# Kernel optimization log

Hardware: AMD Instinct MI355X
Metric: run time of the kernel (lower is better)

The kernel has to match this reference:

```python
import jax, jax.numpy as jnp
import numpy as np

K = 64                 # count_bins
HID = 32               # hidden width of conditioner MLP
PARAM_DIM = 4 * K - 1  # widths(K) + heights(K) + derivs(K-1) + lambdas(K)
BOUND = 3.0
MIN_BIN_W = 1e-3
MIN_BIN_H = 1e-3
MIN_DERIV = 1e-3
N = 1_048_576


def setup_inputs() -> dict:
    key = jax.random.key(0)
    ks = jax.random.split(key, 5)

    def init_lin(k, fan_in, fan_out):
        bnd = 1.0 / np.sqrt(fan_in)
        kw, kb = jax.random.split(k)
        W = jax.random.uniform(kw, (fan_in, fan_out), jnp.float32, -bnd, bnd)
        b = jax.random.uniform(kb, (fan_out,), jnp.float32, -bnd, bnd)
        return W, b

    W1, b1 = init_lin(ks[0], 1, HID)
    W2, b2 = init_lin(ks[1], HID, HID)
    W3, b3 = init_lin(ks[2], HID, PARAM_DIM)
    x = jax.random.normal(ks[3], (N,), jnp.float32)
    condx = jax.random.normal(ks[4], (N,), jnp.float32)
    return {"x": x, "condx": condx, "W1": W1, "b1": b1,
            "W2": W2, "b2": b2, "W3": W3, "b3": b3}


def _normalize_bins(un, min_frac, n):
    # softmax widths -> cumulative knots on [-BOUND, BOUND]
    w = min_frac + (1.0 - min_frac * K) * jax.nn.softmax(un, axis=-1)
    cum = jnp.concatenate([jnp.zeros((n, 1), un.dtype), jnp.cumsum(w, -1)], -1)
    cum = 2.0 * BOUND * cum - BOUND
    cum = cum.at[:, 0].set(-BOUND).at[:, -1].set(BOUND)
    return cum, cum[:, 1:] - cum[:, :-1]


def _spline(x, params):
    # monotonic linear-rational spline (pyro order='linear'), elementwise on x
    n = x.shape[0]
    w_un = params[:, :K]
    h_un = params[:, K:2 * K]
    d_un = params[:, 2 * K:3 * K - 1]
    l_un = params[:, 3 * K - 1:]

    cumw, bw = _normalize_bins(w_un, MIN_BIN_W, n)   # knots/widths in x
    cumh, bh = _normalize_bins(h_un, MIN_BIN_H, n)   # knots/heights in y

    one = jnp.ones((n, 1), x.dtype)
    derivs = jnp.concatenate(
        [one, MIN_DERIV + jax.nn.softplus(d_un), one], -1)  # [n, K+1]
    lambdas = 0.95 * jax.nn.sigmoid(l_un) + 0.025            # [n, K]

    inside = (x >= -BOUND) & (x <= BOUND)
    xc = jnp.clip(x, -BOUND, BOUND)
    # bin search: index of bin containing xc
    idx = jnp.clip(jnp.sum(xc[:, None] >= cumw, axis=-1) - 1, 0, K - 1)[:, None]

    g = lambda a, i: jnp.take_along_axis(a, i, axis=-1)[:, 0]
    xk, wk = g(cumw, idx), g(bw, idx)
    yk, hk = g(cumh, idx), g(bh, idx)
    d0, d1 = g(derivs, idx), g(derivs, idx + 1)
    lam = g(lambdas, idx)

    slope = hk / wk
    wb = jnp.sqrt(d0 / d1)                                   # wa == 1
    wc = (lam * d0 + (1.0 - lam) * wb * d1) / slope
    ya, yb = yk, yk + hk
    yc = ((1.0 - lam) * ya + lam * wb * yb) / ((1.0 - lam) + lam * wb)

    theta = (xc - xk) / wk
    left = theta <= lam
    num = jnp.where(left, ya * (lam - theta) + wc * yc * theta,
                    wc * yc * (1.0 - theta) + wb * yb * (theta - lam))
    den = jnp.where(left, (lam - theta) + wc * theta,
                    wc * (1.0 - theta) + wb * (theta - lam))
    y_in = num / den
    dnum = jnp.where(left, wc * lam * (yc - ya),
                     wb * wc * (1.0 - lam) * (yb - yc))
    ld_in = jnp.log(dnum) - 2.0 * jnp.log(jnp.abs(den)) - jnp.log(wk)

    y = jnp.where(inside, y_in, x)       # identity outside support
    ld = jnp.where(inside, ld_in, 0.0)
    return y, ld


def reference(x, condx, W1, b1, W2, b2, W3, b3):
    # conditioner MLP: cond scalar -> 4K-1 unnormalized spline params
    h = jax.nn.relu(condx[:, None] @ W1 + b1)
    h = jax.nn.relu(h @ W2 + b2)
    params = h @ W3 + b3                 # [N, 4K-1]
    y, logdet = _spline(x, params)
    return y, logdet
```

## Files before the change

### kernel.cpp

```cpp
#include <hip/hip_runtime.h>
#include <math.h>

#define BOUND 3.0f
#define LOG2E 1.4426950408889634f
#define LN2 0.6931471805599453f
#define CINV 0.17806267806267807f

typedef _Float16 half8 __attribute__((ext_vector_type(8)));
typedef _Float16 half4 __attribute__((ext_vector_type(4)));
typedef _Float16 half2v __attribute__((ext_vector_type(2)));
typedef float f32x4 __attribute__((ext_vector_type(4)));

__device__ __forceinline__ float fexp2(float x) { return __builtin_amdgcn_exp2f(x); }
__device__ __forceinline__ float flog2(float x) { return __builtin_amdgcn_logf(x); }
__device__ __forceinline__ float frcp(float x)  { return __builtin_amdgcn_rcpf(x); }

__device__ __forceinline__ float hsum2(half2v a, float c) {
    const half2v ones = {(_Float16)1.f, (_Float16)1.f};
    return __builtin_amdgcn_fdot2(a, ones, c, false);
}

__global__ void prep_kernel(const float* __restrict__ W2, const float* __restrict__ W3,
                            const float* __restrict__ b3,
                            _Float16* __restrict__ aW2, _Float16* __restrict__ aW3,
                            float* __restrict__ b3s) {
    int tid = blockIdx.x * blockDim.x + threadIdx.x;
    int nth = gridDim.x * blockDim.x;
    for (int i = tid; i < 16 * 64 * 8; i += nth) {
        int t = i & 7, l = (i >> 3) & 63, m = i >> 9;
        int k = 8 * (l >> 4) + t, col = 16 * m + (l & 15);
        float v = (col < 255) ? W3[k * 255 + col] : 0.f;
        if (m < 8) v *= LOG2E;
        aW3[i] = (_Float16)v;
    }
    for (int i = tid; i < 2 * 64 * 8; i += nth) {
        int t = i & 7, l = (i >> 3) & 63, m = i >> 9;
        int k = 8 * (l >> 4) + t, col = 16 * m + (l & 15);
        aW2[i] = (_Float16)W2[k * 32 + col];
    }
    for (int i = tid; i < 255; i += nth)
        b3s[i] = b3[i] * ((i < 128) ? LOG2E : 1.f);
}

__global__ __launch_bounds__(64, 2) void spline_kernel(
    const float* __restrict__ x_in, const float* __restrict__ cond_in,
    const float* __restrict__ W1, const float* __restrict__ b1,
    const float* __restrict__ b2, const float* __restrict__ b3s,
    const _Float16* __restrict__ aW2, const _Float16* __restrict__ aW3,
    float* __restrict__ out, int N) {

    __shared__ float sbuf[64 * 64];
    __shared__ float scx[64];

    const int l = threadIdx.x;
    const int j = l & 15, g = l >> 4;
    const int sx = l & 7;
    const int ksw = j & 7;
    const int gown = blockIdx.x * 64 + l;
    const int ic = (gown < N) ? gown : (N - 1);

    float* buf = sbuf;
    _Float16* bufh = (_Float16*)sbuf;

    scx[l] = cond_in[ic];
    float x = x_in[ic];

    float4 w1a = *(const float4*)(W1 + 8 * g);
    float4 w1b = *(const float4*)(W1 + 8 * g + 4);
    float4 b1a = *(const float4*)(b1 + 8 * g);
    float4 b1b = *(const float4*)(b1 + 8 * g + 4);

    half8 h1hi[4], h1lo[4];
#pragma unroll
    for (int n = 0; n < 4; n++) {
        float c = scx[16 * n + j];
        float h[8];
        h[0] = fmaxf(fmaf(c, w1a.x, b1a.x), 0.f);
        h[1] = fmaxf(fmaf(c, w1a.y, b1a.y), 0.f);
        h[2] = fmaxf(fmaf(c, w1a.z, b1a.z), 0.f);
        h[3] = fmaxf(fmaf(c, w1a.w, b1a.w), 0.f);
        h[4] = fmaxf(fmaf(c, w1b.x, b1b.x), 0.f);
        h[5] = fmaxf(fmaf(c, w1b.y, b1b.y), 0.f);
        h[6] = fmaxf(fmaf(c, w1b.z, b1b.z), 0.f);
        h[7] = fmaxf(fmaf(c, w1b.w, b1b.w), 0.f);
#pragma unroll
        for (int t = 0; t < 8; t++) {
            _Float16 hi = (_Float16)h[t];
            h1hi[n][t] = hi;
            h1lo[n][t] = (_Float16)(h[t] - (float)hi);
        }
    }

    half8 a2[2];
    a2[0] = *(const half8*)(aW2 + (0 * 64 + l) * 8);
    a2[1] = *(const half8*)(aW2 + (1 * 64 + l) * 8);

#pragma unroll
    for (int m = 0; m < 2; m++) {
        float4 bb = *(const float4*)(b2 + 16 * m + 4 * g);
        f32x4 binit = {bb.x, bb.y, bb.z, bb.w};
#pragma unroll
        for (int n = 0; n < 4; n++) {
            f32x4 acc = binit;
            acc = __builtin_amdgcn_mfma_f32_16x16x32_f16(a2[m], h1lo[n], acc, 0, 0, 0);
            acc = __builtin_amdgcn_mfma_f32_16x16x32_f16(a2[m], h1hi[n], acc, 0, 0, 0);
            float v0 = fmaxf(acc[0], 0.f), v1 = fmaxf(acc[1], 0.f);
            float v2 = fmaxf(acc[2], 0.f), v3 = fmaxf(acc[3], 0.f);
            _Float16 p0 = (_Float16)v0, p1 = (_Float16)v1, p2 = (_Float16)v2, p3 = (_Float16)v3;
            half4 hv = {p0, p1, p2, p3};
            half4 lv = {(_Float16)(v0 - (float)p0), (_Float16)(v1 - (float)p1),
                        (_Float16)(v2 - (float)p2), (_Float16)(v3 - (float)p3)};
            int rb = (16 * n + j) * 64;
            *(half4*)(bufh + rb + (((2 * m + (g >> 1)) ^ ksw) << 3) + ((g & 1) << 2)) = hv;
            *(half4*)(bufh + rb + (((4 + 2 * m + (g >> 1)) ^ ksw) << 3) + ((g & 1) << 2)) = lv;
        }
    }

    half8 bhi[4], blo[4];
#pragma unroll
    for (int n = 0; n < 4; n++) {
        int rb = (16 * n + j) * 64;
        bhi[n] = *(const half8*)(bufh + rb + ((g ^ ksw) << 3));
        blo[n] = *(const half8*)(bufh + rb + (((4 + g) ^ ksw) << 3));
    }

    bool inside = (x >= -BOUND) && (x <= BOUND);
    float xc = fminf(fmaxf(x, -BOUND), BOUND);

#pragma unroll
    for (int m = 0; m < 4; m++) {
        half8 a = *(const half8*)(aW3 + (m * 64 + l) * 8);
        float4 bb = *(const float4*)(b3s + 16 * m + 4 * g);
        f32x4 binit = {bb.x, bb.y, bb.z, bb.w};
#pragma unroll
        for (int n = 0; n < 4; n++) {
            f32x4 acc = binit;
            acc = __builtin_amdgcn_mfma_f32_16x16x32_f16(a, blo[n], acc, 0, 0, 0);
            acc = __builtin_amdgcn_mfma_f32_16x16x32_f16(a, bhi[n], acc, 0, 0, 0);
            f32x4 e = {fexp2(acc[0]), fexp2(acc[1]), fexp2(acc[2]), fexp2(acc[3])};
            *(f32x4*)(buf + (16 * n + j) * 64 + (((4 * m + g) ^ ksw) << 2)) = e;
        }
    }

    int idx; float idxf, xk, wk;
    {
        f32x4 wv[16];
#pragma unroll
        for (int t = 0; t < 16; t++)
            wv[t] = *(const f32x4*)(buf + l * 64 + (((t ^ sx)) << 2));
        float G[16];
        float run = 0.f;
#pragma unroll
        for (int t = 0; t < 16; t++) {
            run += (wv[t][0] + wv[t][1]) + (wv[t][2] + wv[t][3]);
            G[t] = run;
        }
        float tot = G[15];
        float rcptot = frcp(tot);
        float rr = (xc + BOUND) * tot * CINV;
        float dr1 = 0.0010683761f * tot;
        float dr4 = 4.f * dr1;
        float r = rr, Gsel = 0.f;
        int qidx = 0;
#pragma unroll
        for (int t = 0; t < 15; t++) {
            r -= dr4;
            bool c = (G[t] <= r);
            qidx += c ? 1 : 0;
            Gsel = c ? G[t] : Gsel;
        }
        f32x4 fv = wv[0];
#pragma unroll
        for (int t = 1; t < 16; t++) fv = (qidx == t) ? wv[t] : fv;
        float e0 = fv[0], e1 = fv[1], e2 = fv[2], e3 = fv[3];
        float qf = (float)qidx;
        float rq = fmaf(-qf, dr4, rr);
        float p1 = Gsel + e0, p2 = p1 + e1, p3 = p2 + e2;
        bool c1 = (p1 <= rq - dr1);
        bool c2 = (p2 <= fmaf(-2.f, dr1, rq));
        bool c3 = (p3 <= fmaf(-3.f, dr1, rq));
        idx = 4 * qidx + (c1 ? 1 : 0) + (c2 ? 1 : 0) + (c3 ? 1 : 0);
        float Pk = c1 ? p1 : Gsel; Pk = c2 ? p2 : Pk; Pk = c3 ? p3 : Pk;
        float ek = c1 ? e1 : e0;   ek = c2 ? e2 : ek; ek = c3 ? e3 : ek;
        idxf = (float)idx;
        xk = fmaf(0.006f, idxf, -BOUND) + 5.616f * Pk * rcptot;
        wk = fmaf(5.616f * rcptot, ek, 0.006f);
        wk = (idx == 63) ? (BOUND - xk) : wk;
    }

#pragma unroll
    for (int m = 0; m < 4; m++) {
        half8 a = *(const half8*)(aW3 + ((m + 4) * 64 + l) * 8);
        float4 bb = *(const float4*)(b3s + 64 + 16 * m + 4 * g);
        f32x4 binit = {bb.x, bb.y, bb.z, bb.w};
#pragma unroll
        for (int n = 0; n < 4; n++) {
            f32x4 acc = binit;
            acc = __builtin_amdgcn_mfma_f32_16x16x32_f16(a, bhi[n], acc, 0, 0, 0);
            half4 e = {(_Float16)fexp2(acc[0]), (_Float16)fexp2(acc[1]),
                       (_Float16)fexp2(acc[2]), (_Float16)fexp2(acc[3])};
            *(half4*)(bufh + (16 * n + j) * 64 +
                      (((2 * m + (g >> 1)) ^ ksw) << 3) + ((g & 1) << 2)) = e;
        }
    }

    float yk, hk;
    {
        int qh = idx >> 2, rh = idx & 3;
        float toth = 0.f, Gq = 0.f;
#pragma unroll
        for (int t = 0; t < 8; t++) {
            half8 hv = *(const half8*)(bufh + l * 64 + ((t ^ sx) << 3));
            half2v* hp = (half2v*)&hv;
            float gs0 = hsum2(hp[0], hsum2(hp[1], 0.f));
            float gs1 = hsum2(hp[2], hsum2(hp[3], 0.f));
            toth += gs0 + gs1;
            Gq += (2 * t < qh) ? gs0 : 0.f;
            Gq += (2 * t + 1 < qh) ? gs1 : 0.f;
        }
        half4 fv = *(const half4*)(bufh + l * 64 + (((qh >> 1) ^ sx) << 3) + ((qh & 1) << 2));
        float f0 = (float)fv[0], f1 = (float)fv[1], f2 = (float)fv[2], f3 = (float)fv[3];
        float Sh = Gq;
        Sh += (rh >= 1) ? f0 : 0.f;
        Sh += (rh >= 2) ? f1 : 0.f;
        Sh += (rh >= 3) ? f2 : 0.f;
        float x01 = (rh & 1) ? f1 : f0;
        float x23 = (rh & 1) ? f3 : f2;
        float eidx = (rh & 2) ? x23 : x01;
        float chh = 5.616f * frcp(toth);
        yk = fmaf(0.006f, idxf, -BOUND) + chh * Sh;
        hk = fmaf(chh, eidx, 0.006f);
        hk = (idx == 63) ? (BOUND - yk) : hk;
    }

    int c0 = (idx > 0) ? (idx - 1) : 0;
    float accd0, accd1, accl;
    {
#pragma unroll
        for (int m = 0; m < 4; m++) {
            half8 a = *(const half8*)(aW3 + ((m + 8) * 64 + l) * 8);
#pragma unroll
            for (int n = 0; n < 4; n++) {
                f32x4 acc = {0.f, 0.f, 0.f, 0.f};
                acc = __builtin_amdgcn_mfma_f32_16x16x32_f16(a, bhi[n], acc, 0, 0, 0);
                *(f32x4*)(buf + (16 * n + j) * 64 + (((4 * m + g) ^ ksw) << 2)) = acc;
            }
        }
        accd0 = buf[l * 64 + (((c0 >> 2) ^ sx) << 2) + (c0 & 3)];
        accd1 = buf[l * 64 + (((idx >> 2) ^ sx) << 2) + (idx & 3)];
        float acl0 = buf[l * 64 + ((15 ^ sx) << 2) + 3];
#pragma unroll
        for (int m = 0; m < 4; m++) {
            half8 a = *(const half8*)(aW3 + ((m + 12) * 64 + l) * 8);
#pragma unroll
            for (int n = 0; n < 4; n++) {
                f32x4 acc = {0.f, 0.f, 0.f, 0.f};
                acc = __builtin_amdgcn_mfma_f32_16x16x32_f16(a, bhi[n], acc, 0, 0, 0);
                *(f32x4*)(buf + (16 * n + j) * 64 + (((4 * m + g) ^ ksw) << 2)) = acc;
            }
        }
        float aclB = buf[l * 64 + (((c0 >> 2) ^ sx) << 2) + (c0 & 3)];
        accd0 += b3s[127 + idx];
        accd1 += b3s[(idx < 63) ? (128 + idx) : 191];
        accl = ((idx == 0) ? acl0 : aclB) + b3s[191 + idx];
    }

    float e0t = fexp2(-fabsf(accd0) * LOG2E);
    float sp0 = fmaxf(accd0, 0.f) + LN2 * flog2(1.f + e0t);
    float e1t = fexp2(-fabsf(accd1) * LOG2E);
    float sp1 = fmaxf(accd1, 0.f) + LN2 * flog2(1.f + e1t);
    float d0 = (idx == 0)  ? 1.f : (0.001f + sp0);
    float d1 = (idx == 63) ? 1.f : (0.001f + sp1);
    float sig = frcp(1.f + fexp2(-accl * LOG2E));
    float lam = fmaf(0.95f, sig, 0.025f);

    float rwk = frcp(wk);
    float wb = sqrtf(d0 * frcp(d1));
    float wc = fmaf(lam, d0, (1.f - lam) * wb * d1) * wk * frcp(hk);
    float ya = yk, yb = yk + hk;
    float yc = fmaf(1.f - lam, ya, lam * wb * yb) * frcp(fmaf(lam, wb, 1.f - lam));
    float theta = (xc - xk) * rwk;
    bool left = theta <= lam;
    float num = left ? fmaf(ya, lam - theta, wc * yc * theta)
                     : fmaf(wc * yc, 1.f - theta, wb * yb * (theta - lam));
    float den = left ? fmaf(wc, theta, lam - theta)
                     : fmaf(wc, 1.f - theta, wb * (theta - lam));
    float y_in = num * frcp(den);
    float dnum = left ? (wc * lam * (yc - ya))
                      : (wb * wc * (1.f - lam) * (yb - yc));
    float ld_in = LN2 * (flog2(dnum) - 2.f * flog2(fabsf(den)) - flog2(wk));

    if (gown < N) {
        out[gown]     = inside ? y_in : x;
        out[N + gown] = inside ? ld_in : 0.f;
    }
}

extern "C" void kernel_launch(void* const* d_in, const int* in_sizes, int n_in,
                              void* d_out, int out_size, void* d_ws, size_t ws_size,
                              hipStream_t stream) {
    const float* x  = (const float*)d_in[0];
    const float* cx = (const float*)d_in[1];
    const float* W1 = (const float*)d_in[2];
    const float* b1 = (const float*)d_in[3];
    const float* W2 = (const float*)d_in[4];
    const float* b2 = (const float*)d_in[5];
    const float* W3 = (const float*)d_in[6];
    const float* b3 = (const float*)d_in[7];
    int N = in_sizes[0];

    _Float16* aW3 = (_Float16*)d_ws;
    _Float16* aW2 = aW3 + 16 * 64 * 8;
    float* b3s = (float*)(aW2 + 2 * 64 * 8);
    float* out = (float*)d_out;

    hipLaunchKernelGGL(prep_kernel, dim3(8), dim3(256), 0, stream, W2, W3, b3, aW2, aW3, b3s);
    hipLaunchKernelGGL(spline_kernel, dim3((N + 63) / 64), dim3(64), 0, stream,
                       x, cx, W1, b1, b2, b3s, aW2, aW3, out, N);
}
```

Baseline: 64.28 us.

## Halve shared staging buffer and raise occupancy to four waves per SIMD

Shrinks the per-block shared-memory staging buffer from 64x64 to 64x32 floats by processing the third-layer MFMA outputs in two or four half-width passes and reading each half back before it is overwritten. The cond broadcast now uses a wave shuffle instead of shared memory. Launch bounds are raised from 2 to 4 waves to improve latency hiding. In exchange there are extra LDS round trips and selects, and the tighter register budget may cause spills, since wv[16] now stays live across the passes.

```diff
diff --git a/kernel.cpp b/kernel.cpp
--- a/kernel.cpp
+++ b/kernel.cpp
@@ -42,15 +42,14 @@
         b3s[i] = b3[i] * ((i < 128) ? LOG2E : 1.f);
 }
 
-__global__ __launch_bounds__(64, 2) void spline_kernel(
+__global__ __launch_bounds__(64, 4) void spline_kernel(
     const float* __restrict__ x_in, const float* __restrict__ cond_in,
     const float* __restrict__ W1, const float* __restrict__ b1,
     const float* __restrict__ b2, const float* __restrict__ b3s,
     const _Float16* __restrict__ aW2, const _Float16* __restrict__ aW3,
     float* __restrict__ out, int N) {
 
-    __shared__ float sbuf[64 * 64];
-    __shared__ float scx[64];
+    __shared__ float sbuf[64 * 32];
 
     const int l = threadIdx.x;
     const int j = l & 15, g = l >> 4;
@@ -62,7 +61,7 @@
     float* buf = sbuf;
     _Float16* bufh = (_Float16*)sbuf;
 
-    scx[l] = cond_in[ic];
+    float cx = cond_in[ic];
     float x = x_in[ic];
 
     float4 w1a = *(const float4*)(W1 + 8 * g);
@@ -73,7 +72,7 @@
     half8 h1hi[4], h1lo[4];
 #pragma unroll
     for (int n = 0; n < 4; n++) {
-        float c = scx[16 * n + j];
+        float c = __shfl(cx, 16 * n + j, 64);
         float h[8];
         h[0] = fmaxf(fmaf(c, w1a.x, b1a.x), 0.f);
         h[1] = fmaxf(fmaf(c, w1a.y, b1a.y), 0.f);
@@ -127,27 +126,31 @@
     bool inside = (x >= -BOUND) && (x <= BOUND);
     float xc = fminf(fmaxf(x, -BOUND), BOUND);
 
-#pragma unroll
-    for (int m = 0; m < 4; m++) {
-        half8 a = *(const half8*)(aW3 + (m * 64 + l) * 8);
-        float4 bb = *(const float4*)(b3s + 16 * m + 4 * g);
-        f32x4 binit = {bb.x, bb.y, bb.z, bb.w};
-#pragma unroll
-        for (int n = 0; n < 4; n++) {
-            f32x4 acc = binit;
-            acc = __builtin_amdgcn_mfma_f32_16x16x32_f16(a, blo[n], acc, 0, 0, 0);
-            acc = __builtin_amdgcn_mfma_f32_16x16x32_f16(a, bhi[n], acc, 0, 0, 0);
-            f32x4 e = {fexp2(acc[0]), fexp2(acc[1]), fexp2(acc[2]), fexp2(acc[3])};
-            *(f32x4*)(buf + (16 * n + j) * 64 + (((4 * m + g) ^ ksw) << 2)) = e;
-        }
+    f32x4 wv[16];
+#pragma unroll
+    for (int s = 0; s < 2; s++) {
+#pragma unroll
+        for (int mm = 0; mm < 2; mm++) {
+            int m = 2 * s + mm;
+            half8 a = *(const half8*)(aW3 + (m * 64 + l) * 8);
+            float4 bb = *(const float4*)(b3s + 16 * m + 4 * g);
+            f32x4 binit = {bb.x, bb.y, bb.z, bb.w};
+#pragma unroll
+            for (int n = 0; n < 4; n++) {
+                f32x4 acc = binit;
+                acc = __builtin_amdgcn_mfma_f32_16x16x32_f16(a, blo[n], acc, 0, 0, 0);
+                acc = __builtin_amdgcn_mfma_f32_16x16x32_f16(a, bhi[n], acc, 0, 0, 0);
+                f32x4 e = {fexp2(acc[0]), fexp2(acc[1]), fexp2(acc[2]), fexp2(acc[3])};
+                *(f32x4*)(buf + (16 * n + j) * 32 + (((4 * mm + g) ^ ksw) << 2)) = e;
+            }
+        }
+#pragma unroll
+        for (int t = 0; t < 8; t++)
+            wv[8 * s + t] = *(const f32x4*)(buf + l * 32 + ((t ^ sx) << 2));
     }
 
     int idx; float idxf, xk, wk;
     {
-        f32x4 wv[16];
-#pragma unroll
-        for (int t = 0; t < 16; t++)
-            wv[t] = *(const f32x4*)(buf + l * 64 + (((t ^ sx)) << 2));
         float G[16];
         float run = 0.f;
 #pragma unroll
@@ -233,37 +236,41 @@
         hk = (idx == 63) ? (BOUND - yk) : hk;
     }
 
-    int c0 = (idx > 0) ? (idx - 1) : 0;
-    float accd0, accd1, accl;
-    {
-#pragma unroll
-        for (int m = 0; m < 4; m++) {
-            half8 a = *(const half8*)(aW3 + ((m + 8) * 64 + l) * 8);
+    const int c0 = (idx > 0) ? (idx - 1) : 0;
+    const int rc0a = (c0 < 32) ? c0 : 31;
+    const int rc0b = (c0 >= 32) ? (c0 - 32) : 0;
+    const int rc1a = (idx < 32) ? idx : 31;
+    const int rc1b = (idx >= 32) ? (idx - 32) : 0;
+    float v0a, v0b, v1a, v1b, vl191, vla, vlb;
+#pragma unroll
+    for (int s = 0; s < 4; s++) {
+#pragma unroll
+        for (int mm = 0; mm < 2; mm++) {
+            half8 a = *(const half8*)(aW3 + ((8 + 2 * s + mm) * 64 + l) * 8);
 #pragma unroll
             for (int n = 0; n < 4; n++) {
                 f32x4 acc = {0.f, 0.f, 0.f, 0.f};
                 acc = __builtin_amdgcn_mfma_f32_16x16x32_f16(a, bhi[n], acc, 0, 0, 0);
-                *(f32x4*)(buf + (16 * n + j) * 64 + (((4 * m + g) ^ ksw) << 2)) = acc;
+                *(f32x4*)(buf + (16 * n + j) * 32 + (((4 * mm + g) ^ ksw) << 2)) = acc;
             }
         }
-        accd0 = buf[l * 64 + (((c0 >> 2) ^ sx) << 2) + (c0 & 3)];
-        accd1 = buf[l * 64 + (((idx >> 2) ^ sx) << 2) + (idx & 3)];
-        float acl0 = buf[l * 64 + ((15 ^ sx) << 2) + 3];
-#pragma unroll
-        for (int m = 0; m < 4; m++) {
-            half8 a = *(const half8*)(aW3 + ((m + 12) * 64 + l) * 8);
-#pragma unroll
-            for (int n = 0; n < 4; n++) {
-                f32x4 acc = {0.f, 0.f, 0.f, 0.f};
-                acc = __builtin_amdgcn_mfma_f32_16x16x32_f16(a, bhi[n], acc, 0, 0, 0);
-                *(f32x4*)(buf + (16 * n + j) * 64 + (((4 * m + g) ^ ksw) << 2)) = acc;
-            }
-        }
-        float aclB = buf[l * 64 + (((c0 >> 2) ^ sx) << 2) + (c0 & 3)];
-        accd0 += b3s[127 + idx];
-        accd1 += b3s[(idx < 63) ? (128 + idx) : 191];
-        accl = ((idx == 0) ? acl0 : aclB) + b3s[191 + idx];
-    }
+        if (s == 0) {
+            v0a = buf[l * 32 + (((rc0a >> 2) ^ sx) << 2) + (rc0a & 3)];
+            v1a = buf[l * 32 + (((rc1a >> 2) ^ sx) << 2) + (rc1a & 3)];
+        } else if (s == 1) {
+            v0b = buf[l * 32 + (((rc0b >> 2) ^ sx) << 2) + (rc0b & 3)];
+            v1b = buf[l * 32 + (((rc1b >> 2) ^ sx) << 2) + (rc1b & 3)];
+            vl191 = buf[l * 32 + ((7 ^ sx) << 2) + 3];
+        } else if (s == 2) {
+            vla = buf[l * 32 + (((rc0a >> 2) ^ sx) << 2) + (rc0a & 3)];
+        } else {
+            vlb = buf[l * 32 + (((rc0b >> 2) ^ sx) << 2) + (rc0b & 3)];
+        }
+    }
+    float accd0 = ((c0 < 32) ? v0a : v0b) + b3s[127 + idx];
+    float accd1 = ((idx < 32) ? v1a : v1b) + b3s[(idx < 63) ? (128 + idx) : 191];
+    float lsel = (c0 < 32) ? vla : vlb;
+    float accl = ((idx == 0) ? vl191 : lsel) + b3s[191 + idx];
 
     float e0t = fexp2(-fabsf(accd0) * LOG2E);
     float sp0 = fmaxf(accd0, 0.f) + LN2 * flog2(1.f + e0t);
```

Measured after the change: 59.43 us. 7.5% less time.
